# Kernel tuning notes

Measured on AMD Instinct MI355X. Metric: run time of the kernel, lower is better.

## Reference

```python
import jax, jax.numpy as jnp
import numpy as np

N_NODES = 50000
N_EDGES = 800000
N_GRAPHS = 2000
N_PAIRS = 4096
IN_CH = 64
EMB = 128
HID = 256
OUT = 1


def gcn_conv(x, edge_index, W, b):
    # PyG GCNConv: h = x @ W^T, then D^{-1/2}(A+I)D^{-1/2} h + b
    h = x @ W.T                                  # [N, out]
    row, col = edge_index[0], edge_index[1]
    ones = jnp.ones((edge_index.shape[1],), h.dtype)
    deg = jax.ops.segment_sum(ones, col, num_segments=N_NODES) + 1.0  # self-loop
    dinv = jax.lax.rsqrt(deg)
    norm = dinv[row] * dinv[col]                 # [E]
    agg = jax.ops.segment_sum(h[row] * norm[:, None], col, num_segments=N_NODES)
    agg = agg + h * (1.0 / deg)[:, None]         # self-loop term (dinv[i]^2)
    return agg + b


def setup_inputs() -> dict:
    key = jax.random.key(0)
    ks = jax.random.split(key, 10)
    x = jax.random.normal(ks[0], (N_NODES, IN_CH), jnp.float32)
    edge_index = jax.random.randint(ks[1], (2, N_EDGES), 0, N_NODES, jnp.int64)
    batch = jnp.sort(jax.random.randint(ks[2], (N_NODES,), 0, N_GRAPHS, jnp.int64))
    drug_drug_batch = jax.random.randint(ks[3], (2, N_PAIRS), 0, N_GRAPHS, jnp.int64)

    def xavier(k, shape):
        fan_out, fan_in = shape
        lim = jnp.sqrt(6.0 / (fan_in + fan_out))
        return jax.random.uniform(k, shape, jnp.float32, -lim, lim)

    return {
        "x": x, "edge_index": edge_index, "batch": batch,
        "drug_drug_batch": drug_drug_batch,
        "conv1_w": xavier(ks[4], (EMB, IN_CH)), "conv1_b": jnp.zeros((EMB,), jnp.float32),
        "conv2_w": xavier(ks[5], (EMB, EMB)), "conv2_b": jnp.zeros((EMB,), jnp.float32),
        "reg1_w": xavier(ks[6], (HID, 2 * EMB)), "reg1_b": jnp.zeros((HID,), jnp.float32),
        "reg2_w": xavier(ks[7], (OUT, HID)), "reg2_b": jnp.zeros((OUT,), jnp.float32),
    }


def reference(x, edge_index, batch, drug_drug_batch,
              conv1_w, conv1_b, conv2_w, conv2_b,
              reg1_w, reg1_b, reg2_w, reg2_b):
    h = jax.nn.relu(gcn_conv(x, edge_index, conv1_w, conv1_b))
    h = jax.nn.relu(gcn_conv(h, edge_index, conv2_w, conv2_b))

    # scatter_mean readout over graphs
    gsum = jax.ops.segment_sum(h, batch, num_segments=N_GRAPHS)
    cnt = jax.ops.segment_sum(jnp.ones((N_NODES,), h.dtype), batch, num_segments=N_GRAPHS)
    graph_embeds = gsum / jnp.maximum(cnt, 1.0)[:, None]

    # quantize drug ids to dense graph indices (np.digitize on unique+1, as in source)
    dd = np.asarray(drug_drug_batch)
    bins = np.unique(dd.flatten()) + 1
    q = jnp.asarray(np.digitize(dd, bins))       # [2, P]

    pairs = jnp.concatenate([graph_embeds[q[0]], graph_embeds[q[1]]], axis=1)  # [P, 2*EMB]
    out = jax.nn.relu(pairs @ reg1_w.T + reg1_b)
    return out @ reg2_w.T + reg2_b
```

## Files before the change

kernel.cpp:

```cpp
#include <hip/hip_runtime.h>

#define N_NODES  50000
#define N_PAD    50048
#define N_EDGES  800000
#define N_GRAPHS 2000
#define N_PAIRS  4096
#define IN_CH    64
#define EMB      128
#define HID      256
#define PPB      16
#define DPAD     16

__device__ inline int wave_incl_scan(int x, int lane) {
    #pragma unroll
    for (int off = 1; off < 64; off <<= 1) {
        int y = __shfl_up(x, off, 64);
        if (lane >= off) x += y;
    }
    return x;
}

__global__ void k_zero_dig(float4* __restrict__ p, int n4,
                           const int* __restrict__ dd, int* __restrict__ rankx) {
    int nzb = (n4 + 255) >> 8;
    int t = threadIdx.x, lane = t & 63, wid = t >> 6;
    if ((int)blockIdx.x < nzb) {
        int i = blockIdx.x * 256 + t;
        if (i < n4) p[i] = make_float4(0.f, 0.f, 0.f, 0.f);
    } else {
        __shared__ int pres[N_GRAPHS];
        __shared__ int ws2[4];
        __shared__ int carry;
        for (int i = t; i < N_GRAPHS; i += 256) pres[i] = 0;
        __syncthreads();
        for (int i = t; i < 2 * N_PAIRS; i += 256) pres[dd[i]] = 1;
        if (t == 0) carry = 0;
        __syncthreads();
        for (int base = 0; base < N_GRAPHS; base += 256) {
            int i = base + t;
            int v = (i < N_GRAPHS) ? pres[i] : 0;
            int x = wave_incl_scan(v, lane);
            if (lane == 63) ws2[wid] = x;
            __syncthreads();
            int add = carry;
            for (int w = 0; w < wid; ++w) add += ws2[w];
            if (i < N_GRAPHS) rankx[i] = x - v + add;
            __syncthreads();
            if (t == 255) carry = add + x;
            __syncthreads();
        }
    }
}

__global__ void k_pre(const int* __restrict__ col, const int* __restrict__ batch,
                      const float* __restrict__ w1, const float* __restrict__ w2,
                      int* __restrict__ deg, int* __restrict__ pos_e, int* __restrict__ cnt,
                      float* __restrict__ wt1, float* __restrict__ wt2) {
    int e = blockIdx.x * 256 + threadIdx.x;
    if (e < N_EDGES) {
        int c = col[e];
        pos_e[e] = atomicAdd(&deg[c * DPAD], 1);
    }
    if (e < N_NODES) atomicAdd(&cnt[batch[e]], 1);
    if (e < EMB * IN_CH) {
        int j = e / IN_CH, k = e % IN_CH;
        wt1[k * EMB + j] = w1[e];
    } else if (e < EMB * IN_CH + EMB * EMB) {
        int t = e - EMB * IN_CH;
        int j = t / EMB, k = t % EMB;
        wt2[k * EMB + j] = w2[t];
    }
}

__global__ void k_scan1(const int* __restrict__ in, int* __restrict__ part, int n) {
    __shared__ int ws[4];
    int i = blockIdx.x * 256 + threadIdx.x;
    int lane = threadIdx.x & 63, wid = threadIdx.x >> 6;
    int v = (i < n) ? in[i * DPAD] : 0;
    int x = wave_incl_scan(v, lane);
    if (lane == 63) ws[wid] = x;
    __syncthreads();
    if (threadIdx.x == 0) part[blockIdx.x] = ws[0] + ws[1] + ws[2] + ws[3];
}

__global__ void k_scan3d(const int* __restrict__ in, const int* __restrict__ part,
                         int* __restrict__ off, float* __restrict__ dinv) {
    __shared__ int ws[4];
    __shared__ int psum[4];
    int t = threadIdx.x;
    int lane = t & 63, wid = t >> 6;
    int pp = 0;
    for (int w = t; w < (int)blockIdx.x; w += 256) pp += part[w];
    #pragma unroll
    for (int o = 32; o > 0; o >>= 1) pp += __shfl_down(pp, o, 64);
    if (lane == 0) psum[wid] = pp;
    int i = blockIdx.x * 256 + t;
    int v = (i < N_NODES) ? in[i * DPAD] : 0;
    int x = wave_incl_scan(v, lane);
    if (lane == 63) ws[wid] = x;
    __syncthreads();
    int add = psum[0] + psum[1] + psum[2] + psum[3];
    for (int w = 0; w < wid; ++w) add += ws[w];
    if (i < N_NODES) {
        off[i] = x - v + add;
        dinv[i] = 1.0f / sqrtf((float)(v + 1));
    }
    if (i == 0) off[N_NODES] = N_EDGES;
}

__global__ void k_fill_scale(const int* __restrict__ row, const int* __restrict__ col,
                             const int* __restrict__ pos_e, const int* __restrict__ off,
                             int* __restrict__ csr_row,
                             const float4* __restrict__ x, const float* __restrict__ dinv,
                             float4* __restrict__ xs) {
    int idx = blockIdx.x * 256 + threadIdx.x;
    if (idx < N_EDGES) {
        int c = col[idx];
        int p = pos_e[idx];
        csr_row[off[c] + p] = row[idx];
    } else {
        int i = idx - N_EDGES;
        int n = i >> 4;
        float d = dinv[n];
        float4 v = x[i];
        v.x *= d; v.y *= d; v.z *= d; v.w *= d;
        xs[i] = v;
    }
}

__device__ inline void f4add(float4& a, const float4 b) {
    a.x += b.x; a.y += b.y; a.z += b.z; a.w += b.w;
}

__global__ __launch_bounds__(256) void k_conv1f(
        const float4* __restrict__ xs, const int* __restrict__ csr_row,
        const int* __restrict__ off, const float* __restrict__ dinv,
        const float* __restrict__ w1t, const float* __restrict__ b1,
        float* __restrict__ h1s) {
    __shared__ __align__(16) float a_lds[32 * IN_CH];
    int t = threadIdx.x;
    int base = blockIdx.x * 32;
    {
        int c4l = t & 7;
        int nl = t >> 3;
        int n = base + nl;
        int s = 0, e = 0;
        float dn = 0.f;
        if (n < N_NODES) { s = off[n]; e = off[n + 1]; dn = dinv[n]; }
        #pragma unroll
        for (int g = 0; g < 2; ++g) {
            int c4 = c4l + g * 8;
            float4 acc = make_float4(0.f, 0.f, 0.f, 0.f);
            if (n < N_NODES) {
                acc = xs[n * 16 + c4];
                int i = s;
                for (; i + 8 <= e; i += 8) {
                    int r0 = csr_row[i + 0], r1 = csr_row[i + 1], r2 = csr_row[i + 2], r3 = csr_row[i + 3];
                    int r4 = csr_row[i + 4], r5 = csr_row[i + 5], r6 = csr_row[i + 6], r7 = csr_row[i + 7];
                    float4 a0 = xs[r0 * 16 + c4], a1 = xs[r1 * 16 + c4];
                    float4 a2 = xs[r2 * 16 + c4], a3 = xs[r3 * 16 + c4];
                    float4 a4 = xs[r4 * 16 + c4], a5 = xs[r5 * 16 + c4];
                    float4 a6 = xs[r6 * 16 + c4], a7 = xs[r7 * 16 + c4];
                    f4add(a0, a1); f4add(a2, a3); f4add(a4, a5); f4add(a6, a7);
                    f4add(a0, a2); f4add(a4, a6);
                    f4add(a0, a4);
                    f4add(acc, a0);
                }
                for (; i < e; ++i) {
                    float4 a = xs[csr_row[i] * 16 + c4];
                    f4add(acc, a);
                }
                acc.x *= dn; acc.y *= dn; acc.z *= dn; acc.w *= dn;
            }
            *reinterpret_cast<float4*>(&a_lds[nl * IN_CH + c4 * 4]) = acc;
        }
    }
    __syncthreads();
    {
        int cq = (t & 31) << 2;
        int rg = t >> 5;
        float4 acc[4];
        #pragma unroll
        for (int r = 0; r < 4; ++r) acc[r] = make_float4(0.f, 0.f, 0.f, 0.f);
        #pragma unroll 2
        for (int k = 0; k < IN_CH; k += 4) {
            float4 w0 = *reinterpret_cast<const float4*>(&w1t[(k + 0) * EMB + cq]);
            float4 w1 = *reinterpret_cast<const float4*>(&w1t[(k + 1) * EMB + cq]);
            float4 w2 = *reinterpret_cast<const float4*>(&w1t[(k + 2) * EMB + cq]);
            float4 w3 = *reinterpret_cast<const float4*>(&w1t[(k + 3) * EMB + cq]);
            #pragma unroll
            for (int r = 0; r < 4; ++r) {
                float4 a = *reinterpret_cast<const float4*>(&a_lds[(rg * 4 + r) * IN_CH + k]);
                acc[r].x = fmaf(a.x, w0.x, fmaf(a.y, w1.x, fmaf(a.z, w2.x, fmaf(a.w, w3.x, acc[r].x))));
                acc[r].y = fmaf(a.x, w0.y, fmaf(a.y, w1.y, fmaf(a.z, w2.y, fmaf(a.w, w3.y, acc[r].y))));
                acc[r].z = fmaf(a.x, w0.z, fmaf(a.y, w1.z, fmaf(a.z, w2.z, fmaf(a.w, w3.z, acc[r].z))));
                acc[r].w = fmaf(a.x, w0.w, fmaf(a.y, w1.w, fmaf(a.z, w2.w, fmaf(a.w, w3.w, acc[r].w))));
            }
        }
        float4 bv = *reinterpret_cast<const float4*>(&b1[cq]);
        #pragma unroll
        for (int r = 0; r < 4; ++r) {
            int row = base + rg * 4 + r;
            if (row < N_NODES) {
                float4 v = acc[r];
                v.x += bv.x; v.y += bv.y; v.z += bv.z; v.w += bv.w;
                float sc = dinv[row];
                v.x = fmaxf(v.x, 0.f) * sc; v.y = fmaxf(v.y, 0.f) * sc;
                v.z = fmaxf(v.z, 0.f) * sc; v.w = fmaxf(v.w, 0.f) * sc;
                *reinterpret_cast<float4*>(&h1s[(size_t)row * EMB + cq]) = v;
            }
        }
    }
}

template <int K>
__global__ void k_gemmv5(const float* __restrict__ A, const float* __restrict__ Wt,
                         float* __restrict__ out) {
    __shared__ __align__(16) float a_lds[64 * K];
    int t = threadIdx.x;
    {
        const float4* Ag = reinterpret_cast<const float4*>(A + (size_t)blockIdx.x * 64 * K);
        float4* Al = reinterpret_cast<float4*>(a_lds);
        constexpr int NV = (64 * K) / (4 * 256);
        #pragma unroll
        for (int i = 0; i < NV; ++i) Al[t + i * 256] = Ag[t + i * 256];
    }
    __syncthreads();
    int cq = (t & 31) << 2;
    int rg = t >> 5;
    float4 acc[8];
    #pragma unroll
    for (int r = 0; r < 8; ++r) acc[r] = make_float4(0.f, 0.f, 0.f, 0.f);
    #pragma unroll 2
    for (int k = 0; k < K; k += 4) {
        float4 w0 = *reinterpret_cast<const float4*>(&Wt[(k + 0) * EMB + cq]);
        float4 w1 = *reinterpret_cast<const float4*>(&Wt[(k + 1) * EMB + cq]);
        float4 w2 = *reinterpret_cast<const float4*>(&Wt[(k + 2) * EMB + cq]);
        float4 w3 = *reinterpret_cast<const float4*>(&Wt[(k + 3) * EMB + cq]);
        #pragma unroll
        for (int r = 0; r < 8; ++r) {
            float4 a = *reinterpret_cast<const float4*>(&a_lds[(rg * 8 + r) * K + k]);
            acc[r].x = fmaf(a.x, w0.x, fmaf(a.y, w1.x, fmaf(a.z, w2.x, fmaf(a.w, w3.x, acc[r].x))));
            acc[r].y = fmaf(a.x, w0.y, fmaf(a.y, w1.y, fmaf(a.z, w2.y, fmaf(a.w, w3.y, acc[r].y))));
            acc[r].z = fmaf(a.x, w0.z, fmaf(a.y, w1.z, fmaf(a.z, w2.z, fmaf(a.w, w3.z, acc[r].z))));
            acc[r].w = fmaf(a.x, w0.w, fmaf(a.y, w1.w, fmaf(a.z, w2.w, fmaf(a.w, w3.w, acc[r].w))));
        }
    }
    int row0 = blockIdx.x * 64 + rg * 8;
    #pragma unroll
    for (int r = 0; r < 8; ++r) {
        int row = row0 + r;
        if (row < N_NODES) {
            *reinterpret_cast<float4*>(&out[(size_t)row * EMB + cq]) = acc[r];
        }
    }
}

template <int HALF>
__global__ void k_gro_h(const float4* __restrict__ t2, const int* __restrict__ csr_row,
                        const int* __restrict__ off, const float* __restrict__ dinv,
                        const float* __restrict__ bias, const int* __restrict__ batch,
                        float* __restrict__ gsum) {
    constexpr int NPB = 16;
    __shared__ __align__(16) float hb[NPB][64];
    __shared__ int bg[NPB];
    int t = threadIdx.x;
    int local = t >> 4;
    int c4 = t & 15;
    int n0 = blockIdx.x * NPB;
    int n = n0 + local;
    if (t < NPB) bg[t] = batch[n0 + t];
    int s = off[n], e = off[n + 1];
    const int cidx = HALF * 16 + c4;
    float4 acc = t2[(size_t)n * 32 + cidx];
    int i = s;
    for (; i + 8 <= e; i += 8) {
        int r0 = csr_row[i + 0], r1 = csr_row[i + 1], r2 = csr_row[i + 2], r3 = csr_row[i + 3];
        int r4 = csr_row[i + 4], r5 = csr_row[i + 5], r6 = csr_row[i + 6], r7 = csr_row[i + 7];
        float4 a0 = t2[(size_t)r0 * 32 + cidx], a1 = t2[(size_t)r1 * 32 + cidx];
        float4 a2 = t2[(size_t)r2 * 32 + cidx], a3 = t2[(size_t)r3 * 32 + cidx];
        float4 a4 = t2[(size_t)r4 * 32 + cidx], a5 = t2[(size_t)r5 * 32 + cidx];
        float4 a6 = t2[(size_t)r6 * 32 + cidx], a7 = t2[(size_t)r7 * 32 + cidx];
        f4add(a0, a1); f4add(a2, a3); f4add(a4, a5); f4add(a6, a7);
        f4add(a0, a2); f4add(a4, a6);
        f4add(a0, a4);
        f4add(acc, a0);
    }
    for (; i < e; ++i) {
        float4 a = t2[(size_t)csr_row[i] * 32 + cidx];
        f4add(acc, a);
    }
    float dn = dinv[n];
    float4 b = reinterpret_cast<const float4*>(bias)[cidx];
    acc.x = fmaxf(fmaf(acc.x, dn, b.x), 0.f);
    acc.y = fmaxf(fmaf(acc.y, dn, b.y), 0.f);
    acc.z = fmaxf(fmaf(acc.z, dn, b.z), 0.f);
    acc.w = fmaxf(fmaf(acc.w, dn, b.w), 0.f);
    *reinterpret_cast<float4*>(&hb[local][c4 * 4]) = acc;
    __syncthreads();
    {
        int ch = t & 63, q = t >> 6;
        int j0 = q * 4;
        int g = bg[j0];
        float a = 0.f;
        #pragma unroll
        for (int j = j0; j < j0 + 4; ++j) {
            int gj = bg[j];
            if (gj != g) { atomicAdd(&gsum[g * EMB + HALF * 64 + ch], a); a = 0.f; g = gj; }
            a += hb[j][ch];
        }
        atomicAdd(&gsum[g * EMB + HALF * 64 + ch], a);
    }
}

__global__ void k_mlp16(const float* __restrict__ gemb, const int* __restrict__ cnt,
                        const int* __restrict__ dd, const int* __restrict__ rankx,
                        const float* __restrict__ w1, const float* __restrict__ b1,
                        const float* __restrict__ w2, const float* __restrict__ b2,
                        float* __restrict__ out) {
    __shared__ __align__(16) float pv[PPB][2 * EMB];
    __shared__ float wpart[4][PPB];
    int p0 = blockIdx.x * PPB;
    int t = threadIdx.x;
    int lane = t & 63, wid = t >> 6;
    #pragma unroll
    for (int j = 0; j < PPB; ++j) {
        int p = p0 + j;
        if (t < EMB) {
            int ga = rankx[dd[p]];
            int ca = cnt[ga];
            float ra = 1.0f / (float)(ca > 1 ? ca : 1);
            pv[j][t] = gemb[ga * EMB + t] * ra;
        } else {
            int gb = rankx[dd[N_PAIRS + p]];
            int cb = cnt[gb];
            float rb = 1.0f / (float)(cb > 1 ? cb : 1);
            pv[j][t] = gemb[gb * EMB + (t - EMB)] * rb;
        }
    }
    __syncthreads();
    float acc[PPB];
    float bv = b1[t];
    #pragma unroll
    for (int j = 0; j < PPB; ++j) acc[j] = bv;
    const float4* wrow = reinterpret_cast<const float4*>(&w1[t * 2 * EMB]);
    for (int k = 0; k < (2 * EMB) / 4; ++k) {
        float4 w = wrow[k];
        #pragma unroll
        for (int j = 0; j < PPB; ++j) {
            const float4 xv = *reinterpret_cast<const float4*>(&pv[j][k * 4]);
            acc[j] = fmaf(xv.x, w.x, fmaf(xv.y, w.y, fmaf(xv.z, w.z, fmaf(xv.w, w.w, acc[j]))));
        }
    }
    float w2t = w2[t];
    float contrib[PPB];
    #pragma unroll
    for (int j = 0; j < PPB; ++j) contrib[j] = fmaxf(acc[j], 0.f) * w2t;
    #pragma unroll
    for (int off = 32; off > 0; off >>= 1) {
        #pragma unroll
        for (int j = 0; j < PPB; ++j) contrib[j] += __shfl_down(contrib[j], off, 64);
    }
    if (lane == 0) {
        #pragma unroll
        for (int j = 0; j < PPB; ++j) wpart[wid][j] = contrib[j];
    }
    __syncthreads();
    if (t < PPB) {
        out[p0 + t] = wpart[0][t] + wpart[1][t] + wpart[2][t] + wpart[3][t] + b2[0];
    }
}

extern "C" void kernel_launch(void* const* d_in, const int* in_sizes, int n_in,
                              void* d_out, int out_size, void* d_ws, size_t ws_size,
                              hipStream_t stream) {
    const float* x        = (const float*)d_in[0];
    const int*   ei       = (const int*)d_in[1];
    const int*   batch    = (const int*)d_in[2];
    const int*   dd       = (const int*)d_in[3];
    const float* conv1_w  = (const float*)d_in[4];
    const float* conv1_b  = (const float*)d_in[5];
    const float* conv2_w  = (const float*)d_in[6];
    const float* conv2_b  = (const float*)d_in[7];
    const float* reg1_w   = (const float*)d_in[8];
    const float* reg1_b   = (const float*)d_in[9];
    const float* reg2_w   = (const float*)d_in[10];
    const float* reg2_b   = (const float*)d_in[11];
    float* outp = (float*)d_out;

    const int* ei_row = ei;
    const int* ei_col = ei + N_EDGES;

    char* ws = (char*)d_ws;
    size_t o = 0;
    auto alloc = [&](size_t bytes) -> void* {
        void* p = ws + o;
        o = (o + bytes + 255) & ~(size_t)255;
        return p;
    };
    size_t zero_start = o;
    int*   deg     = (int*)alloc((size_t)N_NODES * DPAD * 4);
    int*   cnt     = (int*)alloc(N_GRAPHS * 4);
    float* gsum    = (float*)alloc(N_GRAPHS * EMB * 4);
    size_t zero_bytes = o - zero_start;
    int*   off     = (int*)alloc((N_NODES + 1) * 4);
    float* dinv    = (float*)alloc(N_NODES * 4);
    int*   part    = (int*)alloc(256 * 4);
    int*   pos_e   = (int*)alloc(N_EDGES * 4);
    int*   csr_row = (int*)alloc(N_EDGES * 4);
    int*   rankx   = (int*)alloc(N_GRAPHS * 4);
    float* Wt1     = (float*)alloc(IN_CH * EMB * 4);
    float* Wt2     = (float*)alloc(EMB * EMB * 4);
    float* h1s     = (float*)alloc((size_t)N_PAD * EMB * 4);
    float* t2      = (float*)alloc((size_t)N_PAD * EMB * 4);
    float* xs      = t2;

    (void)ws_size; (void)in_sizes; (void)n_in; (void)out_size;

    {
        int n4 = (int)(zero_bytes / 16);
        int nzb = (n4 + 255) / 256;
        k_zero_dig<<<nzb + 1, 256, 0, stream>>>((float4*)(ws + zero_start), n4, dd, rankx);
    }

    k_pre<<<N_EDGES / 256, 256, 0, stream>>>(ei_col, batch, conv1_w, conv2_w,
                                             deg, pos_e, cnt, Wt1, Wt2);
    {
        int nb = (N_NODES + 255) / 256;
        k_scan1<<<nb, 256, 0, stream>>>(deg, part, N_NODES);
        k_scan3d<<<nb, 256, 0, stream>>>(deg, part, off, dinv);
    }
    k_fill_scale<<<(N_EDGES + N_NODES * (IN_CH / 4)) / 256, 256, 0, stream>>>(
        ei_row, ei_col, pos_e, off, csr_row, (const float4*)x, dinv, (float4*)xs);

    k_conv1f<<<N_PAD / 32, 256, 0, stream>>>(
        (const float4*)xs, csr_row, off, dinv, Wt1, conv1_b, h1s);

    k_gemmv5<EMB><<<N_PAD / 64, 256, 0, stream>>>(h1s, Wt2, t2);
    k_gro_h<0><<<N_NODES / 16, 256, 0, stream>>>(
        (const float4*)t2, csr_row, off, dinv, conv2_b, batch, gsum);
    k_gro_h<1><<<N_NODES / 16, 256, 0, stream>>>(
        (const float4*)t2, csr_row, off, dinv, conv2_b, batch, gsum);

    k_mlp16<<<N_PAIRS / PPB, 256, 0, stream>>>(gsum, cnt, dd, rankx,
                                               reg1_w, reg1_b, reg2_w, reg2_b, outp);
}
```

Measured before the change: 227.2 us.

## Merge conv2 gather halves into one launch and move dig/gsum-zero into k_pre

```diff
diff --git a/kernel.cpp b/kernel.cpp
--- a/kernel.cpp
+++ b/kernel.cpp
@@ -10,6 +10,7 @@
 #define HID      256
 #define PPB      16
 #define DPAD     16
+#define GROB     1563
 
 __device__ inline int wave_incl_scan(int x, int lane) {
     #pragma unroll
@@ -20,17 +21,36 @@
     return x;
 }
 
-__global__ void k_zero_dig(float4* __restrict__ p, int n4,
-                           const int* __restrict__ dd, int* __restrict__ rankx) {
-    int nzb = (n4 + 255) >> 8;
-    int t = threadIdx.x, lane = t & 63, wid = t >> 6;
-    if ((int)blockIdx.x < nzb) {
-        int i = blockIdx.x * 256 + t;
-        if (i < n4) p[i] = make_float4(0.f, 0.f, 0.f, 0.f);
-    } else {
+__global__ void k_zero(float4* __restrict__ p, int n4) {
+    int i = blockIdx.x * 256 + threadIdx.x;
+    if (i < n4) p[i] = make_float4(0.f, 0.f, 0.f, 0.f);
+}
+
+__global__ void k_pre(const int* __restrict__ col, const int* __restrict__ batch,
+                      const float* __restrict__ w1, const float* __restrict__ w2,
+                      int* __restrict__ deg, int* __restrict__ pos_e, int* __restrict__ cnt,
+                      float* __restrict__ wt1, float* __restrict__ wt2,
+                      const int* __restrict__ dd, int* __restrict__ rankx,
+                      float4* __restrict__ gsum4) {
+    int b = blockIdx.x, t = threadIdx.x;
+    if (b < N_EDGES / 256) {
+        int e = b * 256 + t;
+        int c = col[e];
+        pos_e[e] = atomicAdd(&deg[c * DPAD], 1);
+        if (e < N_NODES) atomicAdd(&cnt[batch[e]], 1);
+        if (e < EMB * IN_CH) {
+            int j = e / IN_CH, k = e % IN_CH;
+            wt1[k * EMB + j] = w1[e];
+        } else if (e < EMB * IN_CH + EMB * EMB) {
+            int q = e - EMB * IN_CH;
+            int j = q / EMB, k = q % EMB;
+            wt2[k * EMB + j] = w2[q];
+        }
+    } else if (b == N_EDGES / 256) {
         __shared__ int pres[N_GRAPHS];
         __shared__ int ws2[4];
         __shared__ int carry;
+        int lane = t & 63, wid = t >> 6;
         for (int i = t; i < N_GRAPHS; i += 256) pres[i] = 0;
         __syncthreads();
         for (int i = t; i < 2 * N_PAIRS; i += 256) pres[dd[i]] = 1;
@@ -49,26 +69,10 @@
             if (t == 255) carry = add + x;
             __syncthreads();
         }
-    }
-}
-
-__global__ void k_pre(const int* __restrict__ col, const int* __restrict__ batch,
-                      const float* __restrict__ w1, const float* __restrict__ w2,
-                      int* __restrict__ deg, int* __restrict__ pos_e, int* __restrict__ cnt,
-                      float* __restrict__ wt1, float* __restrict__ wt2) {
-    int e = blockIdx.x * 256 + threadIdx.x;
-    if (e < N_EDGES) {
-        int c = col[e];
-        pos_e[e] = atomicAdd(&deg[c * DPAD], 1);
-    }
-    if (e < N_NODES) atomicAdd(&cnt[batch[e]], 1);
-    if (e < EMB * IN_CH) {
-        int j = e / IN_CH, k = e % IN_CH;
-        wt1[k * EMB + j] = w1[e];
-    } else if (e < EMB * IN_CH + EMB * EMB) {
-        int t = e - EMB * IN_CH;
-        int j = t / EMB, k = t % EMB;
-        wt2[k * EMB + j] = w2[t];
+    } else {
+        int i = (b - N_EDGES / 256 - 1) * 256 + t;
+        for (int k = i; k < N_GRAPHS * EMB / 4; k += 4096)
+            gsum4[k] = make_float4(0.f, 0.f, 0.f, 0.f);
     }
 }
 
@@ -256,60 +260,71 @@
     }
 }
 
-template <int HALF>
-__global__ void k_gro_h(const float4* __restrict__ t2, const int* __restrict__ csr_row,
-                        const int* __restrict__ off, const float* __restrict__ dinv,
-                        const float* __restrict__ bias, const int* __restrict__ batch,
-                        float* __restrict__ gsum) {
-    constexpr int NPB = 16;
-    __shared__ __align__(16) float hb[NPB][64];
-    __shared__ int bg[NPB];
+__global__ void k_gro(const float4* __restrict__ t2, const int* __restrict__ csr_row,
+                      const int* __restrict__ off, const float* __restrict__ dinv,
+                      const float* __restrict__ bias, const int* __restrict__ batch,
+                      float* __restrict__ gsum) {
+    __shared__ __align__(16) float hb[32][64];
+    __shared__ int bg[32];
     int t = threadIdx.x;
-    int local = t >> 4;
-    int c4 = t & 15;
-    int n0 = blockIdx.x * NPB;
+    int bid = blockIdx.x;
+    int half = (bid >= GROB) ? 1 : 0;
+    int n0 = (half ? bid - GROB : bid) * 32;
+    int local = t >> 3;
+    int c4l = t & 7;
     int n = n0 + local;
-    if (t < NPB) bg[t] = batch[n0 + t];
-    int s = off[n], e = off[n + 1];
-    const int cidx = HALF * 16 + c4;
-    float4 acc = t2[(size_t)n * 32 + cidx];
-    int i = s;
-    for (; i + 8 <= e; i += 8) {
-        int r0 = csr_row[i + 0], r1 = csr_row[i + 1], r2 = csr_row[i + 2], r3 = csr_row[i + 3];
-        int r4 = csr_row[i + 4], r5 = csr_row[i + 5], r6 = csr_row[i + 6], r7 = csr_row[i + 7];
-        float4 a0 = t2[(size_t)r0 * 32 + cidx], a1 = t2[(size_t)r1 * 32 + cidx];
-        float4 a2 = t2[(size_t)r2 * 32 + cidx], a3 = t2[(size_t)r3 * 32 + cidx];
-        float4 a4 = t2[(size_t)r4 * 32 + cidx], a5 = t2[(size_t)r5 * 32 + cidx];
-        float4 a6 = t2[(size_t)r6 * 32 + cidx], a7 = t2[(size_t)r7 * 32 + cidx];
-        f4add(a0, a1); f4add(a2, a3); f4add(a4, a5); f4add(a6, a7);
-        f4add(a0, a2); f4add(a4, a6);
-        f4add(a0, a4);
-        f4add(acc, a0);
-    }
-    for (; i < e; ++i) {
-        float4 a = t2[(size_t)csr_row[i] * 32 + cidx];
-        f4add(acc, a);
-    }
-    float dn = dinv[n];
-    float4 b = reinterpret_cast<const float4*>(bias)[cidx];
-    acc.x = fmaxf(fmaf(acc.x, dn, b.x), 0.f);
-    acc.y = fmaxf(fmaf(acc.y, dn, b.y), 0.f);
-    acc.z = fmaxf(fmaf(acc.z, dn, b.z), 0.f);
-    acc.w = fmaxf(fmaf(acc.w, dn, b.w), 0.f);
-    *reinterpret_cast<float4*>(&hb[local][c4 * 4]) = acc;
+    if (t < 32) bg[t] = (n0 + t < N_NODES) ? batch[n0 + t] : -1;
+    int s = 0, e = 0;
+    float dn = 0.f;
+    bool valid = (n < N_NODES);
+    if (valid) { s = off[n]; e = off[n + 1]; dn = dinv[n]; }
+    #pragma unroll
+    for (int g = 0; g < 2; ++g) {
+        int cidx = half * 16 + g * 8 + c4l;
+        float4 acc = make_float4(0.f, 0.f, 0.f, 0.f);
+        if (valid) {
+            acc = t2[(size_t)n * 32 + cidx];
+            int i = s;
+            for (; i + 8 <= e; i += 8) {
+                int r0 = csr_row[i + 0], r1 = csr_row[i + 1], r2 = csr_row[i + 2], r3 = csr_row[i + 3];
+                int r4 = csr_row[i + 4], r5 = csr_row[i + 5], r6 = csr_row[i + 6], r7 = csr_row[i + 7];
+                float4 a0 = t2[(size_t)r0 * 32 + cidx], a1 = t2[(size_t)r1 * 32 + cidx];
+                float4 a2 = t2[(size_t)r2 * 32 + cidx], a3 = t2[(size_t)r3 * 32 + cidx];
+                float4 a4 = t2[(size_t)r4 * 32 + cidx], a5 = t2[(size_t)r5 * 32 + cidx];
+                float4 a6 = t2[(size_t)r6 * 32 + cidx], a7 = t2[(size_t)r7 * 32 + cidx];
+                f4add(a0, a1); f4add(a2, a3); f4add(a4, a5); f4add(a6, a7);
+                f4add(a0, a2); f4add(a4, a6);
+                f4add(a0, a4);
+                f4add(acc, a0);
+            }
+            for (; i < e; ++i) {
+                float4 a = t2[(size_t)csr_row[i] * 32 + cidx];
+                f4add(acc, a);
+            }
+            float4 b = reinterpret_cast<const float4*>(bias)[cidx];
+            acc.x = fmaxf(fmaf(acc.x, dn, b.x), 0.f);
+            acc.y = fmaxf(fmaf(acc.y, dn, b.y), 0.f);
+            acc.z = fmaxf(fmaf(acc.z, dn, b.z), 0.f);
+            acc.w = fmaxf(fmaf(acc.w, dn, b.w), 0.f);
+        }
+        *reinterpret_cast<float4*>(&hb[local][(g * 8 + c4l) * 4]) = acc;
+    }
     __syncthreads();
     {
         int ch = t & 63, q = t >> 6;
-        int j0 = q * 4;
+        int j0 = q * 8;
         int g = bg[j0];
-        float a = 0.f;
-        #pragma unroll
-        for (int j = j0; j < j0 + 4; ++j) {
-            int gj = bg[j];
-            if (gj != g) { atomicAdd(&gsum[g * EMB + HALF * 64 + ch], a); a = 0.f; g = gj; }
-            a += hb[j][ch];
-        }
-        atomicAdd(&gsum[g * EMB + HALF * 64 + ch], a);
+        if (g >= 0) {
+            float a = 0.f;
+            #pragma unroll
+            for (int j = j0; j < j0 + 8; ++j) {
+                int gj = bg[j];
+                if (gj < 0) break;
+                if (gj != g) { atomicAdd(&gsum[g * EMB + half * 64 + ch], a); a = 0.f; g = gj; }
+                a += hb[j][ch];
+            }
+            atomicAdd(&gsum[g * EMB + half * 64 + ch], a);
+        }
     }
 }
 
@@ -401,8 +416,8 @@
     size_t zero_start = o;
     int*   deg     = (int*)alloc((size_t)N_NODES * DPAD * 4);
     int*   cnt     = (int*)alloc(N_GRAPHS * 4);
+    size_t zero_bytes = o - zero_start;
     float* gsum    = (float*)alloc(N_GRAPHS * EMB * 4);
-    size_t zero_bytes = o - zero_start;
     int*   off     = (int*)alloc((N_NODES + 1) * 4);
     float* dinv    = (float*)alloc(N_NODES * 4);
     int*   part    = (int*)alloc(256 * 4);
@@ -419,12 +434,12 @@
 
     {
         int n4 = (int)(zero_bytes / 16);
-        int nzb = (n4 + 255) / 256;
-        k_zero_dig<<<nzb + 1, 256, 0, stream>>>((float4*)(ws + zero_start), n4, dd, rankx);
-    }
-
-    k_pre<<<N_EDGES / 256, 256, 0, stream>>>(ei_col, batch, conv1_w, conv2_w,
-                                             deg, pos_e, cnt, Wt1, Wt2);
+        k_zero<<<(n4 + 255) / 256, 256, 0, stream>>>((float4*)(ws + zero_start), n4);
+    }
+
+    k_pre<<<N_EDGES / 256 + 1 + 16, 256, 0, stream>>>(ei_col, batch, conv1_w, conv2_w,
+                                                      deg, pos_e, cnt, Wt1, Wt2,
+                                                      dd, rankx, (float4*)gsum);
     {
         int nb = (N_NODES + 255) / 256;
         k_scan1<<<nb, 256, 0, stream>>>(deg, part, N_NODES);
@@ -437,9 +452,7 @@
         (const float4*)xs, csr_row, off, dinv, Wt1, conv1_b, h1s);
 
     k_gemmv5<EMB><<<N_PAD / 64, 256, 0, stream>>>(h1s, Wt2, t2);
-    k_gro_h<0><<<N_NODES / 16, 256, 0, stream>>>(
-        (const float4*)t2, csr_row, off, dinv, conv2_b, batch, gsum);
-    k_gro_h<1><<<N_NODES / 16, 256, 0, stream>>>(
+    k_gro<<<2 * GROB, 256, 0, stream>>>(
         (const float4*)t2, csr_row, off, dinv, conv2_b, batch, gsum);
 
     k_mlp16<<<N_PAIRS / PPB, 256, 0, stream>>>(gsum, cnt, dd, rankx,
```

New measurement: 216.3 us, median of 2. 4.8% less time.
